# Kernel tuning notes

Hardware: AMD Instinct MI355X
Metric: run time of the kernel (lower is better)

Reference implementation:

```python
import jax, jax.numpy as jnp
import numpy as np

PH, PW = 7, 7            # output_size
SCALE = 0.25             # spatial_scale
SR = 2                   # sampling_ratio
ALIGNED = True


def setup_inputs() -> dict:
    key = jax.random.key(0)
    k1, k2, k3, k4 = jax.random.split(key, 4)
    N, C, H, W = 4, 256, 200, 200
    K = 1000
    x = jax.random.normal(k1, (N, C, H, W), dtype=jnp.float32)
    # boxes in image coordinates (image size = H/SCALE = 800)
    b = jax.random.randint(k2, (K,), 0, N).astype(jnp.float32)
    xy1 = jax.random.uniform(k3, (K, 2), minval=0.0, maxval=600.0)
    wh = jax.random.uniform(k4, (K, 2), minval=8.0, maxval=199.0)
    xy2 = xy1 + wh
    rois = jnp.concatenate([b[:, None], xy1, xy2], axis=1).astype(jnp.float32)
    return {"input": x, "rois": rois}


def _bilinear(img, y, x):
    # img: [C,H,W]; y: [Gy,Gx]; x: [Gy,Gx] -> [C,Gy,Gx]
    C, H, W = img.shape
    valid = (y >= -1.0) & (y <= H) & (x >= -1.0) & (x <= W)
    y = jnp.clip(y, 0.0, H - 1)
    x = jnp.clip(x, 0.0, W - 1)
    y0 = jnp.floor(y).astype(jnp.int32)
    x0 = jnp.floor(x).astype(jnp.int32)
    y1 = jnp.minimum(y0 + 1, H - 1)
    x1 = jnp.minimum(x0 + 1, W - 1)
    ly = y - y0.astype(y.dtype)
    lx = x - x0.astype(x.dtype)
    hy, hx = 1.0 - ly, 1.0 - lx
    v00 = img[:, y0, x0]
    v01 = img[:, y0, x1]
    v10 = img[:, y1, x0]
    v11 = img[:, y1, x1]
    out = (hy * hx) * v00 + (hy * lx) * v01 + (ly * hx) * v10 + (ly * lx) * v11
    return jnp.where(valid[None], out, 0.0)


def _roi_one(feat_all, roi):
    # feat_all: [N,C,H,W]; roi: [5] = (b, x1, y1, x2, y2)
    img = feat_all[roi[0].astype(jnp.int32)]  # [C,H,W]
    C = img.shape[0]
    off = 0.5 if ALIGNED else 0.0
    sx = roi[1] * SCALE - off
    sy = roi[2] * SCALE - off
    rw = (roi[3] - roi[1]) * SCALE
    rh = (roi[4] - roi[2]) * SCALE
    if not ALIGNED:
        rw = jnp.maximum(rw, 1.0)
        rh = jnp.maximum(rh, 1.0)
    bw = rw / PW
    bh = rh / PH
    sub = (jnp.arange(SR, dtype=jnp.float32) + 0.5) / SR  # [SR]
    ys = (sy + (jnp.arange(PH, dtype=jnp.float32)[:, None] + sub[None, :]) * bh).reshape(-1)  # [PH*SR]
    xs = (sx + (jnp.arange(PW, dtype=jnp.float32)[:, None] + sub[None, :]) * bw).reshape(-1)  # [PW*SR]
    Gy, Gx = ys.shape[0], xs.shape[0]
    Y = jnp.broadcast_to(ys[:, None], (Gy, Gx))
    X = jnp.broadcast_to(xs[None, :], (Gy, Gx))
    vals = _bilinear(img, Y, X)  # [C, PH*SR, PW*SR]
    return vals.reshape(C, PH, SR, PW, SR).mean(axis=(2, 4))  # [C,PH,PW]


def reference(input, rois):
    return jax.vmap(_roi_one, in_axes=(None, 0))(input, rois)  # [K,C,PH,PW]
```

## Files before the change

### kernel.cpp

```cpp
#include <hip/hip_runtime.h>
#include <hip/hip_fp16.h>

#define C_    256
#define H_    200
#define W_    200
#define HW    (H_*W_)
#define CHW   ((size_t)C_*HW)
#define PWB   7
#define BINS  49
#define NSMP  196

__global__ __launch_bounds__(256) void nchw_to_nhwc_h(
    const float* __restrict__ in, __half* __restrict__ wsp)
{
    __shared__ float t[64][65];
    const int pgrp = blockIdx.x % 625;
    const int cgrp = (blockIdx.x / 625) & 3;
    const int n    = blockIdx.x / 2500;
    const int p0 = pgrp * 64, c0 = cgrp * 64;
    const int tx = threadIdx.x & 63;
    const int ty = threadIdx.x >> 6;

    const float* src = in + (size_t)n * CHW + (size_t)c0 * HW + p0;
    #pragma unroll
    for (int i = 0; i < 16; ++i) {
        const int c = ty + 4 * i;
        t[tx][c] = src[(size_t)c * HW + tx];
    }
    __syncthreads();
    __half* dst = wsp + (size_t)n * CHW + (size_t)p0 * C_ + c0;
    #pragma unroll
    for (int i = 0; i < 16; ++i) {
        const int p = ty + 4 * i;
        dst[(size_t)p * C_ + tx] = __float2half(t[p][tx]);
    }
}

typedef struct { int o; float w; } OW;
typedef struct __attribute__((aligned(8))) { __half2 a, b; } h4;

__global__ __launch_bounds__(256) void roialign_nhwc_h3(
    const __half* __restrict__ wsp,
    const float* __restrict__ rois,
    float* __restrict__ out,
    int K)
{
    __shared__ OW     s_ow[NSMP][4];
    __shared__ __half s_out[BINS][132];

    const int k    = blockIdx.x % K;
    const int half = blockIdx.x / K;

    const float rx1 = rois[k*5 + 1];
    const float ry1 = rois[k*5 + 2];
    const float rx2 = rois[k*5 + 3];
    const float ry2 = rois[k*5 + 4];
    const int  bidx = (int)rois[k*5 + 0];

    const float sx = __fsub_rn(__fmul_rn(rx1, 0.25f), 0.5f);
    const float sy = __fsub_rn(__fmul_rn(ry1, 0.25f), 0.5f);
    const float bw = __fdiv_rn(__fmul_rn(__fsub_rn(rx2, rx1), 0.25f), 7.0f);
    const float bh = __fdiv_rn(__fmul_rn(__fsub_rn(ry2, ry1), 0.25f), 7.0f);

    const int tid = threadIdx.x;

    if (tid < NSMP) {
        const int bin = tid >> 2, q = tid & 3;
        const int ph = bin / PWB, pw = bin - ph * PWB;
        const float cy = (float)ph + ((q >> 1) ? 0.75f : 0.25f);
        const float cx = (float)pw + ((q & 1)  ? 0.75f : 0.25f);
        const float fy = __fadd_rn(sy, __fmul_rn(cy, bh));
        const float fx = __fadd_rn(sx, __fmul_rn(cx, bw));

        const bool valid = (fy >= -1.0f) && (fy <= (float)H_) &&
                           (fx >= -1.0f) && (fx <= (float)W_);

        const float y = fminf(fmaxf(fy, 0.0f), (float)(H_ - 1));
        const float x = fminf(fmaxf(fx, 0.0f), (float)(W_ - 1));
        const int y0 = (int)floorf(y);
        const int x0 = (int)floorf(x);
        const int y1 = min(y0 + 1, H_ - 1);
        const int x1 = min(x0 + 1, W_ - 1);
        const float ly = y - (float)y0;
        const float lx = x - (float)x0;
        const float hy = 1.0f - ly, hx = 1.0f - lx;

        float w00 = hy*hx, w01 = hy*lx, w10 = ly*hx, w11 = ly*lx;
        if (!valid) { w00 = w01 = w10 = w11 = 0.0f; }

        s_ow[tid][0].o = y0 * W_ + x0;  s_ow[tid][0].w = w00;
        s_ow[tid][1].o = y0 * W_ + x1;  s_ow[tid][1].w = w01;
        s_ow[tid][2].o = y1 * W_ + x0;  s_ow[tid][2].w = w10;
        s_ow[tid][3].o = y1 * W_ + x1;  s_ow[tid][3].w = w11;
    }
    __syncthreads();

    const int wv   = tid >> 6;
    const int lane = tid & 63;
    const int grp  = lane >> 5;
    const int cl4  = lane & 31;
    const h4* __restrict__ img4 =
        (const h4*)(wsp + (size_t)bidx * CHW) + (half * 32 + cl4);

    #pragma unroll 2
    for (int bin = wv; bin < BINS; bin += 4) {
        float a0 = 0, a1 = 0, a2 = 0, a3 = 0;
        #pragma unroll
        for (int j = 0; j < 8; ++j) {
            const int g = j * 2 + grp;
            const OW ow = s_ow[bin * 4 + (g >> 2)][g & 3];
            const h4 f = img4[(size_t)ow.o * 64];
            const float2 flo = __half22float2(f.a);
            const float2 fhi = __half22float2(f.b);
            a0 = fmaf(ow.w, flo.x, a0);
            a1 = fmaf(ow.w, flo.y, a1);
            a2 = fmaf(ow.w, fhi.x, a2);
            a3 = fmaf(ow.w, fhi.y, a3);
        }
        a0 += __shfl_xor(a0, 32);
        a1 += __shfl_xor(a1, 32);
        a2 += __shfl_xor(a2, 32);
        a3 += __shfl_xor(a3, 32);
        if (grp == 0) {
            __half2* dst = (__half2*)&s_out[bin][4 * cl4];
            dst[0] = __floats2half2_rn(a0 * 0.25f, a1 * 0.25f);
            dst[1] = __floats2half2_rn(a2 * 0.25f, a3 * 0.25f);
        }
    }
    __syncthreads();

    float* __restrict__ ob = out + ((size_t)k * C_ + half * 128) * BINS;
    #pragma unroll 1
    for (int e = tid; e < 128 * BINS; e += 256) {
        const int ch = e / BINS, bn = e - ch * BINS;
        ob[e] = __half2float(s_out[bn][ch]);
    }
}

#define CSPLIT 4
#define CB     (C_/CSPLIT)
#define NCG    5
typedef struct __attribute__((aligned(4))) { float x, y; } f2u;

__global__ __launch_bounds__(256) void roialign_fwd_fb(
    const float* __restrict__ input, const float* __restrict__ rois,
    float* __restrict__ out, int K)
{
    const int k  = blockIdx.x / CSPLIT;
    const int cs = blockIdx.x - k * CSPLIT;
    if (k >= K) return;
    const int tid = threadIdx.x;
    const int bin = tid % BINS;
    const int cg  = tid / BINS;
    if (cg >= NCG) return;

    const float rx1 = rois[k*5+1], ry1 = rois[k*5+2];
    const float rx2 = rois[k*5+3], ry2 = rois[k*5+4];
    const int  bidx = (int)rois[k*5+0];
    const float sx = __fsub_rn(__fmul_rn(rx1,0.25f),0.5f);
    const float sy = __fsub_rn(__fmul_rn(ry1,0.25f),0.5f);
    const float bw = __fdiv_rn(__fmul_rn(__fsub_rn(rx2,rx1),0.25f),7.0f);
    const float bh = __fdiv_rn(__fmul_rn(__fsub_rn(ry2,ry1),0.25f),7.0f);
    const int ph = bin / PWB, pw = bin - ph * PWB;

    int off0[4], off1[4];
    float wA0[4], wB0[4], wA1[4], wB1[4];
    #pragma unroll
    for (int q = 0; q < 4; ++q) {
        const float cy = (float)ph + ((q >> 1) ? 0.75f : 0.25f);
        const float cx = (float)pw + ((q & 1)  ? 0.75f : 0.25f);
        const float fy = __fadd_rn(sy, __fmul_rn(cy, bh));
        const float fx = __fadd_rn(sx, __fmul_rn(cx, bw));
        const bool valid = (fy >= -1.0f) && (fy <= (float)H_) &&
                           (fx >= -1.0f) && (fx <= (float)W_);
        const float y = fminf(fmaxf(fy, 0.0f), (float)(H_-1));
        const float x = fminf(fmaxf(fx, 0.0f), (float)(W_-1));
        const int y0 = (int)floorf(y);
        const int x0 = (int)floorf(x);
        const int y1 = min(y0 + 1, H_-1);
        const float ly = y - (float)y0, lx = x - (float)x0;
        const float hy = 1.0f - ly, hx = 1.0f - lx;
        float w00 = hy*hx, w01 = hy*lx, w10 = ly*hx, w11 = ly*lx;
        if (!valid) { w00 = w01 = w10 = w11 = 0.0f; }
        const int xb = min(x0, W_-2);
        const bool xcl = (x0 != xb);
        wA0[q] = xcl ? 0.0f : w00;  wB0[q] = xcl ? w00 : w01;
        wA1[q] = xcl ? 0.0f : w10;  wB1[q] = xcl ? w10 : w11;
        off0[q] = y0 * W_ + xb;     off1[q] = y1 * W_ + xb;
    }
    const float* __restrict__ img  = input + ((size_t)bidx*C_ + cs*CB) * HW;
    float* __restrict__       outk = out   + ((size_t)k   *C_ + cs*CB) * BINS;
    #pragma unroll 2
    for (int c = cg; c < CB; c += NCG) {
        const float* __restrict__ ch = img + (size_t)c * HW;
        float acc = 0.0f;
        #pragma unroll
        for (int q = 0; q < 4; ++q) {
            const f2u p0 = *(const f2u*)(ch + off0[q]);
            const f2u p1 = *(const f2u*)(ch + off1[q]);
            acc += wA0[q]*p0.x + wB0[q]*p0.y + wA1[q]*p1.x + wB1[q]*p1.y;
        }
        outk[c * BINS + bin] = acc * 0.25f;
    }
}

extern "C" void kernel_launch(void* const* d_in, const int* in_sizes, int n_in,
                              void* d_out, int out_size, void* d_ws, size_t ws_size,
                              hipStream_t stream) {
    const float* input = (const float*)d_in[0];
    const float* rois  = (const float*)d_in[1];
    float* out = (float*)d_out;
    const int K = in_sizes[1] / 5;
    const int N = in_sizes[0] / (int)CHW;

    const size_t need = (size_t)N * CHW * sizeof(__half);
    if (ws_size >= need) {
        __half* wsp = (__half*)d_ws;
        nchw_to_nhwc_h<<<N * 2500, 256, 0, stream>>>(input, wsp);
        roialign_nhwc_h3<<<K * 2, 256, 0, stream>>>(wsp, rois, out, K);
    } else {
        roialign_fwd_fb<<<K * CSPLIT, 256, 0, stream>>>(input, rois, out, K);
    }
}
```

Measured before the change: 83.09 us.

## Vectorize NHWC transpose stores and process whole ROI per 512-thread block

The transpose kernel now writes four halves per thread as an 8-byte store instead of scalar half stores. This reduces store instruction count and makes the global writes wider. The ROI kernel drops the two-blocks-per-ROI channel split and uses one 512-thread block per ROI. Each lane covers 4 of the 256 channels and accumulates all 16 samples itself, which removes the cross-half shuffle reduction and halves the per-ROI weight setup. The cost is bigger blocks and shared memory per block, fewer blocks in the grid, and fully serial 16-sample loops per lane.

```diff
diff --git a/kernel.cpp b/kernel.cpp
--- a/kernel.cpp
+++ b/kernel.cpp
@@ -10,6 +10,9 @@
 #define BINS  49
 #define NSMP  196
 
+typedef struct __attribute__((aligned(8))) { __half2 a, b; } h4;
+typedef struct { int o; float w; } OW;
+
 __global__ __launch_bounds__(256) void nchw_to_nhwc_h(
     const float* __restrict__ in, __half* __restrict__ wsp)
 {
@@ -18,8 +21,9 @@
     const int cgrp = (blockIdx.x / 625) & 3;
     const int n    = blockIdx.x / 2500;
     const int p0 = pgrp * 64, c0 = cgrp * 64;
-    const int tx = threadIdx.x & 63;
-    const int ty = threadIdx.x >> 6;
+    const int tid = threadIdx.x;
+    const int tx = tid & 63;
+    const int ty = tid >> 6;
 
     const float* src = in + (size_t)n * CHW + (size_t)c0 * HW + p0;
     #pragma unroll
@@ -28,28 +32,30 @@
         t[tx][c] = src[(size_t)c * HW + tx];
     }
     __syncthreads();
+
     __half* dst = wsp + (size_t)n * CHW + (size_t)p0 * C_ + c0;
+    const int u  = tid & 15;
+    const int pr = tid >> 4;
     #pragma unroll
-    for (int i = 0; i < 16; ++i) {
-        const int p = ty + 4 * i;
-        dst[(size_t)p * C_ + tx] = __float2half(t[p][tx]);
-    }
-}
-
-typedef struct { int o; float w; } OW;
-typedef struct __attribute__((aligned(8))) { __half2 a, b; } h4;
-
-__global__ __launch_bounds__(256) void roialign_nhwc_h3(
+    for (int i = 0; i < 4; ++i) {
+        const int p = pr + 16 * i;
+        h4 v;
+        v.a = __floats2half2_rn(t[p][4*u + 0], t[p][4*u + 1]);
+        v.b = __floats2half2_rn(t[p][4*u + 2], t[p][4*u + 3]);
+        *(h4*)&dst[(size_t)p * C_ + 4*u] = v;
+    }
+}
+
+__global__ __launch_bounds__(512, 8) void roialign_nhwc_h4(
     const __half* __restrict__ wsp,
     const float* __restrict__ rois,
     float* __restrict__ out,
     int K)
 {
     __shared__ OW     s_ow[NSMP][4];
-    __shared__ __half s_out[BINS][132];
-
-    const int k    = blockIdx.x % K;
-    const int half = blockIdx.x / K;
+    __shared__ __half s_out[BINS][260];
+
+    const int k = blockIdx.x;
 
     const float rx1 = rois[k*5 + 1];
     const float ry1 = rois[k*5 + 2];
@@ -97,18 +103,14 @@
 
     const int wv   = tid >> 6;
     const int lane = tid & 63;
-    const int grp  = lane >> 5;
-    const int cl4  = lane & 31;
-    const h4* __restrict__ img4 =
-        (const h4*)(wsp + (size_t)bidx * CHW) + (half * 32 + cl4);
-
-    #pragma unroll 2
-    for (int bin = wv; bin < BINS; bin += 4) {
+    const h4* __restrict__ img4 = (const h4*)(wsp + (size_t)bidx * CHW) + lane;
+
+    #pragma unroll 1
+    for (int bin = wv; bin < BINS; bin += 8) {
         float a0 = 0, a1 = 0, a2 = 0, a3 = 0;
         #pragma unroll
-        for (int j = 0; j < 8; ++j) {
-            const int g = j * 2 + grp;
-            const OW ow = s_ow[bin * 4 + (g >> 2)][g & 3];
+        for (int s = 0; s < 16; ++s) {
+            const OW ow = s_ow[bin * 4 + (s >> 2)][s & 3];
             const h4 f = img4[(size_t)ow.o * 64];
             const float2 flo = __half22float2(f.a);
             const float2 fhi = __half22float2(f.b);
@@ -117,21 +119,16 @@
             a2 = fmaf(ow.w, fhi.x, a2);
             a3 = fmaf(ow.w, fhi.y, a3);
         }
-        a0 += __shfl_xor(a0, 32);
-        a1 += __shfl_xor(a1, 32);
-        a2 += __shfl_xor(a2, 32);
-        a3 += __shfl_xor(a3, 32);
-        if (grp == 0) {
-            __half2* dst = (__half2*)&s_out[bin][4 * cl4];
-            dst[0] = __floats2half2_rn(a0 * 0.25f, a1 * 0.25f);
-            dst[1] = __floats2half2_rn(a2 * 0.25f, a3 * 0.25f);
-        }
+        h4 r;
+        r.a = __floats2half2_rn(a0 * 0.25f, a1 * 0.25f);
+        r.b = __floats2half2_rn(a2 * 0.25f, a3 * 0.25f);
+        *(h4*)&s_out[bin][4 * lane] = r;
     }
     __syncthreads();
 
-    float* __restrict__ ob = out + ((size_t)k * C_ + half * 128) * BINS;
+    float* __restrict__ ob = out + (size_t)k * C_ * BINS;
     #pragma unroll 1
-    for (int e = tid; e < 128 * BINS; e += 256) {
+    for (int e = tid; e < C_ * BINS; e += 512) {
         const int ch = e / BINS, bn = e - ch * BINS;
         ob[e] = __half2float(s_out[bn][ch]);
     }
@@ -217,7 +214,7 @@
     if (ws_size >= need) {
         __half* wsp = (__half*)d_ws;
         nchw_to_nhwc_h<<<N * 2500, 256, 0, stream>>>(input, wsp);
-        roialign_nhwc_h3<<<K * 2, 256, 0, stream>>>(wsp, rois, out, K);
+        roialign_nhwc_h4<<<K, 512, 0, stream>>>(wsp, rois, out, K);
     } else {
         roialign_fwd_fb<<<K * CSPLIT, 256, 0, stream>>>(input, rois, out, K);
     }
```

After: 82.92 us. Within noise of the previous version (-0.2%).
